# Optimization experiments

Hardware: AMD Instinct MI355X
Metric: run time of the kernel (lower is better)

Reference implementation:

```python
import jax, jax.numpy as jnp
import numpy as np

N_T, N_M, E, Q = 100000, 20000, 600000, 200000
F_IN, D, L = 256, 128, 2


def setup_inputs() -> dict:
    key = jax.random.key(0)
    ks = jax.random.split(key, 20)
    s = 1.0 / np.sqrt(D)
    inp = {
        "x_thesis": jax.random.normal(ks[0], (N_T, F_IN), jnp.float32),
        "mentor_node_id": jnp.arange(N_M, dtype=jnp.int64) if jax.config.jax_enable_x64 else jnp.arange(N_M, dtype=jnp.int32),
        "edge_src": jax.random.randint(ks[1], (E,), 0, N_T),
        "edge_dst": jax.random.randint(ks[2], (E,), 0, N_M),
        "eli_src": jax.random.randint(ks[3], (Q,), 0, N_T),
        "eli_dst": jax.random.randint(ks[4], (Q,), 0, N_M),
        # encoder params
        "thesis_lin_w": jax.random.normal(ks[5], (D, F_IN), jnp.float32) / np.sqrt(F_IN),
        "thesis_lin_b": jnp.zeros((D,), jnp.float32),
        "prof_emb": jax.random.normal(ks[6], (N_M, D), jnp.float32),
        # SAGEConv params per layer, per edge type (sup: thesis->mentor, rev: mentor->thesis)
        "W_nbr_sup": jax.random.normal(ks[7], (L, D, D), jnp.float32) * s,
        "W_root_sup": jax.random.normal(ks[8], (L, D, D), jnp.float32) * s,
        "b_sup": jnp.zeros((L, D), jnp.float32),
        "W_nbr_rev": jax.random.normal(ks[9], (L, D, D), jnp.float32) * s,
        "W_root_rev": jax.random.normal(ks[10], (L, D, D), jnp.float32) * s,
        "b_rev": jnp.zeros((L, D), jnp.float32),
        # classifier Linear(2*D -> 1)
        "cls_w": jax.random.normal(ks[11], (2 * D,), jnp.float32) * (1.0 / np.sqrt(2 * D)),
        "cls_b": jnp.zeros((), jnp.float32),
    }
    return inp


def reference(x_thesis, mentor_node_id, edge_src, edge_dst, eli_src, eli_dst,
              thesis_lin_w, thesis_lin_b, prof_emb,
              W_nbr_sup, W_root_sup, b_sup, W_nbr_rev, W_root_rev, b_rev,
              cls_w, cls_b):
    n_t = x_thesis.shape[0]
    n_m = prof_emb.shape[0]
    L_ = W_nbr_sup.shape[0]

    # node encoders
    h_t = x_thesis @ thesis_lin_w.T + thesis_lin_b          # [N_T, D]
    h_m = prof_emb[mentor_node_id]                          # [N_M, D]

    ones = jnp.ones(edge_src.shape[0], h_t.dtype)
    deg_m = jnp.maximum(jax.ops.segment_sum(ones, edge_dst, num_segments=n_m), 1.0)[:, None]
    deg_t = jnp.maximum(jax.ops.segment_sum(ones, edge_src, num_segments=n_t), 1.0)[:, None]

    for l in range(L_):
        # mean-aggregate thesis feats onto mentors (supervised_by edges)
        agg_m = jax.ops.segment_sum(h_t[edge_src], edge_dst, num_segments=n_m) / deg_m
        # mean-aggregate mentor feats onto theses (reverse edges)
        agg_t = jax.ops.segment_sum(h_m[edge_dst], edge_src, num_segments=n_t) / deg_t
        new_m = agg_m @ W_nbr_sup[l].T + h_m @ W_root_sup[l].T + b_sup[l]
        new_t = agg_t @ W_nbr_rev[l].T + h_t @ W_root_rev[l].T + b_rev[l]
        if l < L_ - 1:
            new_m = jax.nn.relu(new_m)
            new_t = jax.nn.relu(new_t)
        h_t, h_m = new_t, new_m

    # edge-level classifier: gather endpoints, concat, linear -> scalar per pair
    z = jnp.concatenate([h_t[eli_src], h_m[eli_dst]], axis=-1)  # [Q, 2D]
    return z @ cls_w + cls_b                                     # [Q]
```

## Files before the change

### kernel.cpp

```cpp
#include <hip/hip_runtime.h>
#include <cstdint>
#include <cstddef>

#define D 128
#define F_IN 256

typedef __attribute__((ext_vector_type(8))) short bf16x8;
typedef __attribute__((ext_vector_type(4))) float f32x4;

__device__ __forceinline__ unsigned short f2bs(float f) {
  unsigned int x = __builtin_bit_cast(unsigned int, f);
  x = x + 0x7fffu + ((x >> 16) & 1u);
  return (unsigned short)(x >> 16);
}
__device__ __forceinline__ unsigned pk2(float lo, float hi) {
  return (unsigned)f2bs(lo) | ((unsigned)f2bs(hi) << 16);
}
__device__ __forceinline__ float b2f(unsigned int lo16) {
  unsigned int x = lo16 << 16;
  return __builtin_bit_cast(float, x);
}
__device__ __forceinline__ void gl_lds16v(const void* g, void* l) {
  __builtin_amdgcn_global_load_lds(
      (__attribute__((address_space(1))) void*)g,
      (__attribute__((address_space(3))) void*)l, 16, 0, 0);
}
__device__ __forceinline__ uint4 pack8(float4 a, float4 b) {
  uint4 o;
  o.x = pk2(a.x, a.y); o.y = pk2(a.z, a.w);
  o.z = pk2(b.x, b.y); o.w = pk2(b.z, b.w);
  return o;
}


__global__ __launch_bounds__(256) void prep_k(
    const float* __restrict__ s0, unsigned short* __restrict__ d0, int n0,
    const float* __restrict__ s1, unsigned short* __restrict__ d1, int n1,
    const float* __restrict__ s2, unsigned short* __restrict__ d2, int n2,
    const float* __restrict__ s3, unsigned short* __restrict__ d3, int n3,
    const float* __restrict__ s4, unsigned short* __restrict__ d4, int n4,
    int nbC,
    const float* __restrict__ emb, const int* __restrict__ ids,
    unsigned short* __restrict__ hm, int NM, int nbG,
    const int* __restrict__ esrc, const int* __restrict__ edst,
    int* __restrict__ bktT, int* __restrict__ bktM,
    int E, int SHT, int SHM, int nbA)
{
  int bid = blockIdx.x;
  int tid = threadIdx.x;
  if (bid < nbC) {
    int j = bid * 256 + tid;
    const float* s; unsigned short* d;
    if (j < n0) { s = s0; d = d0; }
    else {
      j -= n0;
      if (j < n1) { s = s1; d = d1; }
      else {
        j -= n1;
        if (j < n2) { s = s2; d = d2; }
        else {
          j -= n2;
          if (j < n3) { s = s3; d = d3; }
          else { j -= n3; if (j >= n4) return; s = s4; d = d4; }
        }
      }
    }
    const float4* sp = (const float4*)(s + (size_t)j * 8);
    *(uint4*)(d + (size_t)j * 8) = pack8(sp[0], sp[1]);
    return;
  }
  bid -= nbC;
  if (bid < nbG) {
    int i = bid * 256 + tid;
    if (i >= NM * 16) return;
    int r = i >> 4, c = (i & 15) * 8;
    const float* s = emb + (size_t)ids[r] * D + c;
    *(uint4*)(hm + (size_t)r * D + c) = pack8(*(const float4*)s, *(const float4*)(s + 4));
    return;
  }
  bid -= nbG;
  __shared__ int sh[256];
  sh[tid] = 0;
  __syncthreads();
  int stride = nbA * 256;
  for (int e = bid * 256 + tid; e < E; e += stride) {
    atomicAdd(&sh[esrc[e] >> SHT], 1);
    atomicAdd(&sh[128 + (edst[e] >> SHM)], 1);
  }
  __syncthreads();
  if (tid < 128) { if (sh[tid]) atomicAdd(&bktT[tid], sh[tid]); }
  else { if (sh[tid]) atomicAdd(&bktM[tid - 128], sh[tid]); }
}


__global__ void a2_scan_k(const int* __restrict__ bktT, int* __restrict__ baseT, int* __restrict__ curT, int BT,
                          const int* __restrict__ bktM, int* __restrict__ baseM, int* __restrict__ curM, int BM) {
  __shared__ int sT[129], sM[129];
  int tid = threadIdx.x;
  if (tid < BT) sT[tid] = bktT[tid];
  if (tid < BM) sM[tid] = bktM[tid];
  __syncthreads();
  if (tid == 0) { int r = 0; for (int i = 0; i < BT; ++i) { int c = sT[i]; sT[i] = r; r += c; } sT[BT] = r; }
  if (tid == 1) { int r = 0; for (int i = 0; i < BM; ++i) { int c = sM[i]; sM[i] = r; r += c; } sM[BM] = r; }
  __syncthreads();
  if (tid <= BT) { baseT[tid] = sT[tid]; if (tid < BT) curT[tid] = sT[tid]; }
  if (tid <= BM) { baseM[tid] = sM[tid]; if (tid < BM) curM[tid] = sM[tid]; }
}


#define CH 4096

__device__ __forceinline__ void a3_body(
    const int* __restrict__ esrc, const int* __restrict__ edst,
    unsigned* __restrict__ partT, unsigned* __restrict__ partM,
    int* __restrict__ curT, int* __restrict__ curM,
    int E, int BT, int BM, int SHT, int SHM, int blk, char* smraw)
{
  unsigned* stT = (unsigned*)smraw;
  unsigned* stM = stT + CH;
  int* hT  = (int*)(stM + CH);
  int* lbT = hT + 128;
  int* lcT = hT + 256;
  int* gbT = hT + 384;
  int* hM  = hT + 512;
  int* lbM = hT + 640;
  int* lcM = hT + 768;
  int* gbM = hT + 896;
  int* st2 = hT + 1024;

  int tid = threadIdx.x;
  int c0 = blk * CH;
  int len = E - c0; if (len > CH) len = CH;

  if (tid < 128) { hT[tid] = 0; hM[tid] = 0; }
  __syncthreads();
  for (int i = tid; i < len; i += 256) {
    atomicAdd(&hT[esrc[c0 + i] >> SHT], 1);
    atomicAdd(&hM[edst[c0 + i] >> SHM], 1);
  }
  __syncthreads();
  int own = (tid < 128) ? hT[tid] : hM[tid - 128];
  st2[tid] = own;
  __syncthreads();
  for (int dd = 1; dd < 128; dd <<= 1) {
    int y = ((tid & 127) >= dd) ? st2[tid - dd] : 0;
    __syncthreads();
    st2[tid] += y;
    __syncthreads();
  }
  int excl = st2[tid] - own;
  if (tid < 128) { lbT[tid] = excl; lcT[tid] = excl; }
  else { lbM[tid - 128] = excl; lcM[tid - 128] = excl; }
  __syncthreads();
  if (tid < BT) { if (hT[tid]) gbT[tid] = atomicAdd(&curT[tid], hT[tid]); }
  if (tid >= 128 && tid - 128 < BM) { int m = tid - 128; if (hM[m]) gbM[m] = atomicAdd(&curM[m], hM[m]); }
  __syncthreads();
  for (int i = tid; i < len; i += 256) {
    unsigned s = (unsigned)esrc[c0 + i], dn = (unsigned)edst[c0 + i];
    int p = atomicAdd(&lcT[s >> SHT], 1);
    stT[p] = (s << 15) | dn;
    int q = atomicAdd(&lcM[dn >> SHM], 1);
    stM[q] = (dn << 17) | s;
  }
  __syncthreads();
  for (int b = 0; b < BT; ++b) {
    int cb = hT[b]; if (!cb) continue;
    int lb = lbT[b]; int gb = gbT[b];
    for (int i = tid; i < cb; i += 256) partT[gb + i] = stT[lb + i];
  }
  for (int b = 0; b < BM; ++b) {
    int cb = hM[b]; if (!cb) continue;
    int lb = lbM[b]; int gb = gbM[b];
    for (int i = tid; i < cb; i += 256) partM[gb + i] = stM[lb + i];
  }
}


__device__ __forceinline__ void enc_body(
    const float* __restrict__ A, const unsigned short* __restrict__ W,
    const float* __restrict__ bias, unsigned short* __restrict__ out, int M,
    int blk, char* smraw)
{
  float* bufA0 = (float*)smraw;
  unsigned short* bufW0 = (unsigned short*)(smraw + 32768);
  const int tid = threadIdx.x;
  const int w = tid >> 6, l = tid & 63;
  const int wr = w >> 1, wc = w & 1;
  const int lr = l & 15, kg = l >> 4;
  const int row0 = blk * 128;
  const int arow = l >> 3;
  const int au = l & 7;
  const int wrow = l >> 2;
  const int wu = l & 3;

  f32x4 acc[4][4] = {};

  auto stage = [&](int st, int bsel) {
    int k0 = st * 32;
    float* bA = bufA0 + bsel * 4096;
    unsigned short* bW = bufW0 + bsel * 4096;
#pragma unroll
    for (int q = 0; q < 4; ++q) {
      int r = w * 32 + q * 8 + arow;
      int gr = row0 + r; if (gr >= M) gr = M - 1;
      int gu = au ^ (r & 7);
      gl_lds16v(A + (size_t)gr * F_IN + k0 + gu * 4, bA + (w * 32 + q * 8) * 32 + l * 4);
    }
#pragma unroll
    for (int q = 0; q < 2; ++q) {
      int r = w * 32 + q * 16 + wrow;
      int gu = wu ^ ((r >> 1) & 3);
      gl_lds16v(W + (size_t)r * F_IN + k0 + gu * 8, bW + (w * 32 + q * 16) * 32 + l * 8);
    }
  };

  stage(0, 0);
#pragma unroll 1
  for (int st = 0; st < F_IN / 32; ++st) {
    if (st < F_IN / 32 - 1) {
      stage(st + 1, (st + 1) & 1);
      __builtin_amdgcn_sched_barrier(0);
      asm volatile("s_waitcnt vmcnt(6)" ::: "memory");
    } else {
      __builtin_amdgcn_sched_barrier(0);
      asm volatile("s_waitcnt vmcnt(0)" ::: "memory");
    }
    __builtin_amdgcn_s_barrier();
    __builtin_amdgcn_sched_barrier(0);
    const float* bA = bufA0 + (st & 1) * 4096;
    const unsigned short* bW = bufW0 + (st & 1) * 4096;
    bf16x8 aF[4], bF[4];
#pragma unroll
    for (int i = 0; i < 4; ++i) {
      int r = wr * 64 + i * 16 + lr;
      const float4* pa = (const float4*)(bA + r * 32);
      float4 v0 = pa[(2 * kg) ^ (r & 7)];
      float4 v1 = pa[(2 * kg + 1) ^ (r & 7)];
      uint4 c = pack8(v0, v1);
      aF[i] = *(bf16x8*)&c;
    }
#pragma unroll
    for (int j = 0; j < 4; ++j) {
      int r = wc * 64 + j * 16 + lr;
      bF[j] = *(const bf16x8*)&bW[r * 32 + ((kg ^ ((r >> 1) & 3)) * 8)];
    }
#pragma unroll
    for (int i = 0; i < 4; ++i)
#pragma unroll
      for (int j = 0; j < 4; ++j)
        acc[i][j] = __builtin_amdgcn_mfma_f32_16x16x32_bf16(aF[i], bF[j], acc[i][j], 0, 0, 0);
    __builtin_amdgcn_sched_barrier(0);
    __builtin_amdgcn_s_barrier();
  }

  __syncthreads();
  float bn[4];
#pragma unroll
  for (int j = 0; j < 4; ++j) bn[j] = bias[wc * 64 + j * 16 + lr];
  unsigned short* ow = (unsigned short*)smraw + w * 4096;
#pragma unroll
  for (int i = 0; i < 4; ++i)
#pragma unroll
    for (int j = 0; j < 4; ++j) {
      f32x4 v = acc[i][j];
#pragma unroll
      for (int r = 0; r < 4; ++r)
        ow[(i * 16 + kg * 4 + r) * 64 + j * 16 + lr] = f2bs(v[r] + bn[j]);
    }
  __syncthreads();
#pragma unroll
  for (int q = 0; q < 8; ++q) {
    int u = q * 64 + l;
    int lrow = u >> 3;
    int cu = (u & 7) * 8;
    int gr = row0 + wr * 64 + lrow;
    if (gr < M)
      *(uint4*)(out + (size_t)gr * D + wc * 64 + cu) = *(const uint4*)&ow[lrow * 64 + cu];
  }
}

__global__ __launch_bounds__(256) void a3enc_k(
    const int* __restrict__ esrc, const int* __restrict__ edst,
    unsigned* __restrict__ partT, unsigned* __restrict__ partM,
    int* __restrict__ curT, int* __restrict__ curM,
    int E, int BT, int BM, int SHT, int SHM, int nbA3,
    const float* __restrict__ A, const unsigned short* __restrict__ W,
    const float* __restrict__ bias, unsigned short* __restrict__ out, int M)
{
  __shared__ char smraw[49152];
  if ((int)blockIdx.x < nbA3)
    a3_body(esrc, edst, partT, partM, curT, curM, E, BT, BM, SHT, SHM, blockIdx.x, smraw);
  else
    enc_body(A, W, bias, out, M, blockIdx.x - nbA3, smraw);
}


#define BCAP 12288

__global__ __launch_bounds__(256) void b_csr_k(
    const unsigned* __restrict__ partT, const int* __restrict__ baseT,
    int* __restrict__ rowT, int* __restrict__ csrT, int NT, int BT, int SHT,
    const unsigned* __restrict__ partM, const int* __restrict__ baseM,
    int* __restrict__ rowM, int* __restrict__ csrM, int NM, int BM, int SHM, int E)
{
  __shared__ int cnt[1024];
  __shared__ int st[256];
  __shared__ unsigned stage[BCAP];

  const unsigned* part; const int* base; int* row; int* csr;
  int N, SH, KS; unsigned PM; int b; bool last;
  if ((int)blockIdx.x < BT) {
    part = partT; base = baseT; row = rowT; csr = csrT;
    N = NT; SH = SHT; KS = 15; PM = 0x7fffu; b = blockIdx.x; last = (b == BT - 1);
  } else {
    part = partM; base = baseM; row = rowM; csr = csrM;
    N = NM; SH = SHM; KS = 17; PM = 0x1ffffu; b = blockIdx.x - BT; last = (b == BM - 1);
  }
  int tid = threadIdx.x;
  int ebeg = base[b], eend = base[b + 1];
  int tot = eend - ebeg;
  int n0 = b << SH;
  int width = 1 << SH;
  int nw = N - n0; if (nw > width) nw = width;
  int seg = (width + 255) >> 8;

  for (int j = 0; j < seg; ++j) { int idx = tid * seg + j; if (idx < nw) cnt[idx] = 0; }
  __syncthreads();
  for (int i = tid; i < tot; i += 256) {
    int k = (int)(part[ebeg + i] >> KS) - n0;
    atomicAdd(&cnt[k], 1);
  }
  __syncthreads();
  int s = 0;
  for (int j = 0; j < seg; ++j) { int idx = tid * seg + j; if (idx < nw) s += cnt[idx]; }
  st[tid] = s;
  __syncthreads();
  for (int dd = 1; dd < 256; dd <<= 1) {
    int y = (tid >= dd) ? st[tid - dd] : 0;
    __syncthreads();
    st[tid] += y;
    __syncthreads();
  }
  int run = st[tid] - s;
  for (int j = 0; j < seg; ++j) {
    int idx = tid * seg + j;
    if (idx < nw) {
      int c = cnt[idx];
      row[n0 + idx] = ebeg + run;
      cnt[idx] = run;
      run += c;
    }
  }
  if (last && tid == 0) row[N] = E;
  __syncthreads();
  if (tot <= BCAP) {
    for (int i = tid; i < tot; i += 256) {
      unsigned p = part[ebeg + i];
      int k = (int)(p >> KS) - n0;
      int pos = atomicAdd(&cnt[k], 1);
      stage[pos] = p & PM;
    }
    __syncthreads();
    for (int i = tid; i < tot; i += 256) csr[ebeg + i] = (int)stage[i];
  } else {
    for (int i = tid; i < tot; i += 256) {
      unsigned p = part[ebeg + i];
      int k = (int)(p >> KS) - n0;
      int pos = atomicAdd(&cnt[k], 1);
      csr[ebeg + pos] = (int)(p & PM);
    }
  }
}


__global__ __launch_bounds__(256) void aggregate3_k(
    const unsigned short* __restrict__ tabM, const int* __restrict__ rowpM,
    const int* __restrict__ idxM, unsigned short* __restrict__ outM, int nM, int nblkM,
    const unsigned short* __restrict__ tabT, const int* __restrict__ rowpT,
    const int* __restrict__ idxT, unsigned short* __restrict__ outT, int nT)
{
  const unsigned short* tab; const int* rowp; const int* idx;
  unsigned short* outp; int n, nodeb;
  if ((int)blockIdx.x < nblkM) {
    tab = tabM; rowp = rowpM; idx = idxM; outp = outM; n = nM;
    nodeb = blockIdx.x * 8;
  } else {
    tab = tabT; rowp = rowpT; idx = idxT; outp = outT; n = nT;
    nodeb = (blockIdx.x - nblkM) * 8;
  }
  const int tid = threadIdx.x;
  const int l = tid & 63;
  const int sub = l >> 5;
  const int half = (l >> 4) & 1;
  const int l16 = l & 15;
  const int node = nodeb + (tid >> 6) * 2 + sub;
  const int nodeC = node < n ? node : n - 1;
  int b = rowp[nodeC];
  int e = rowp[nodeC + 1];
  if (node >= n) e = b;
  const int deg = e - b;
  int nb = (deg + 15) >> 4;
  int onb = __shfl_xor(nb, 32, 64);
  int trip = nb > onb ? nb : onb;
  const unsigned short* tl = tab + l16 * 8;

  float a0 = 0.f, a1 = 0.f, a2 = 0.f, a3 = 0.f;
  float a4 = 0.f, a5 = 0.f, a6 = 0.f, a7 = 0.f;
  for (int t = 0; t < trip; ++t) {
    int base = b + t * 16 + half;
    int pp[8]; bool ok[8];
#pragma unroll
    for (int u = 0; u < 8; ++u) {
      int p = base + 2 * u;
      ok[u] = p < e;
      pp[u] = ok[u] ? idx[p] : 0;
    }
    uint4 vv[8];
#pragma unroll
    for (int u = 0; u < 8; ++u) {
      uint4 z; z.x = 0u; z.y = 0u; z.z = 0u; z.w = 0u;
      vv[u] = z;
      if (ok[u]) vv[u] = *(const uint4*)(tl + (size_t)pp[u] * D);
    }
#pragma unroll
    for (int u = 0; u < 8; ++u) {
      a0 += b2f(vv[u].x & 0xffffu); a1 += b2f(vv[u].x >> 16);
      a2 += b2f(vv[u].y & 0xffffu); a3 += b2f(vv[u].y >> 16);
      a4 += b2f(vv[u].z & 0xffffu); a5 += b2f(vv[u].z >> 16);
      a6 += b2f(vv[u].w & 0xffffu); a7 += b2f(vv[u].w >> 16);
    }
  }
  a0 += __shfl_xor(a0, 16, 64);
  a1 += __shfl_xor(a1, 16, 64);
  a2 += __shfl_xor(a2, 16, 64);
  a3 += __shfl_xor(a3, 16, 64);
  a4 += __shfl_xor(a4, 16, 64);
  a5 += __shfl_xor(a5, 16, 64);
  a6 += __shfl_xor(a6, 16, 64);
  a7 += __shfl_xor(a7, 16, 64);
  if (node < n && half == 0) {
    float inv = 1.0f / (float)(deg > 1 ? deg : 1);
    uint4 o;
    o.x = pk2(a0 * inv, a1 * inv);
    o.y = pk2(a2 * inv, a3 * inv);
    o.z = pk2(a4 * inv, a5 * inv);
    o.w = pk2(a6 * inv, a7 * inv);
    *(uint4*)(outp + (size_t)node * D + l16 * 8) = o;
  }
}


template<bool RELU>
__device__ __forceinline__ void gemm_body(
    const unsigned short* __restrict__ Aop, const unsigned short* __restrict__ WA,
    const unsigned short* __restrict__ Bop, const unsigned short* __restrict__ WB,
    const float* __restrict__ bias, unsigned short* __restrict__ out, int M,
    int blk, char* smraw)
{
  unsigned short* bufA0 = (unsigned short*)smraw;
  unsigned short* bufW0 = (unsigned short*)(smraw + 16384);
  const int tid = threadIdx.x;
  const int w = tid >> 6, l = tid & 63;
  const int wr = w >> 1, wc = w & 1;
  const int lr = l & 15, kg = l >> 4;
  const int row0 = blk * 128;
  const int srow = l >> 2;
  const int su = l & 3;

  f32x4 acc[4][4] = {};

  auto stage = [&](int st, int bsel) {
    const unsigned short* Ap = (st < 4) ? Aop : Bop;
    const unsigned short* Wp = (st < 4) ? WA : WB;
    int k0 = (st & 3) * 32;
    unsigned short* bA = bufA0 + bsel * 4096;
    unsigned short* bW = bufW0 + bsel * 4096;
#pragma unroll
    for (int q = 0; q < 2; ++q) {
      int r = w * 32 + q * 16 + srow;
      int gr = row0 + r; if (gr >= M) gr = M - 1;
      int gu = su ^ ((r >> 1) & 3);
      gl_lds16v(Ap + (size_t)gr * D + k0 + gu * 8, bA + (w * 32 + q * 16) * 32 + l * 8);
      gl_lds16v(Wp + (size_t)r * D + k0 + gu * 8, bW + (w * 32 + q * 16) * 32 + l * 8);
    }
  };

  stage(0, 0);
#pragma unroll 1
  for (int st = 0; st < 8; ++st) {
    if (st < 7) {
      stage(st + 1, (st + 1) & 1);
      __builtin_amdgcn_sched_barrier(0);
      asm volatile("s_waitcnt vmcnt(4)" ::: "memory");
    } else {
      __builtin_amdgcn_sched_barrier(0);
      asm volatile("s_waitcnt vmcnt(0)" ::: "memory");
    }
    __builtin_amdgcn_s_barrier();
    __builtin_amdgcn_sched_barrier(0);
    const unsigned short* bA = bufA0 + (st & 1) * 4096;
    const unsigned short* bW = bufW0 + (st & 1) * 4096;
    bf16x8 aF[4], bF[4];
#pragma unroll
    for (int i = 0; i < 4; ++i) {
      int r = wr * 64 + i * 16 + lr;
      aF[i] = *(const bf16x8*)&bA[r * 32 + ((kg ^ ((r >> 1) & 3)) * 8)];
    }
#pragma unroll
    for (int j = 0; j < 4; ++j) {
      int r = wc * 64 + j * 16 + lr;
      bF[j] = *(const bf16x8*)&bW[r * 32 + ((kg ^ ((r >> 1) & 3)) * 8)];
    }
#pragma unroll
    for (int i = 0; i < 4; ++i)
#pragma unroll
      for (int j = 0; j < 4; ++j)
        acc[i][j] = __builtin_amdgcn_mfma_f32_16x16x32_bf16(aF[i], bF[j], acc[i][j], 0, 0, 0);
    __builtin_amdgcn_sched_barrier(0);
    __builtin_amdgcn_s_barrier();
  }

  __syncthreads();
  float bn[4];
#pragma unroll
  for (int j = 0; j < 4; ++j) bn[j] = bias[wc * 64 + j * 16 + lr];
  unsigned short* ow = (unsigned short*)smraw + w * 4096;
#pragma unroll
  for (int i = 0; i < 4; ++i)
#pragma unroll
    for (int j = 0; j < 4; ++j) {
      f32x4 v = acc[i][j];
#pragma unroll
      for (int r = 0; r < 4; ++r) {
        float x = v[r] + bn[j];
        if (RELU) x = fmaxf(x, 0.f);
        ow[(i * 16 + kg * 4 + r) * 64 + j * 16 + lr] = f2bs(x);
      }
    }
  __syncthreads();
#pragma unroll
  for (int q = 0; q < 8; ++q) {
    int u = q * 64 + l;
    int lrow = u >> 3;
    int cu = (u & 7) * 8;
    int gr = row0 + wr * 64 + lrow;
    if (gr < M)
      *(uint4*)(out + (size_t)gr * D + wc * 64 + cu) = *(const uint4*)&ow[lrow * 64 + cu];
  }
}

template<bool RELU>
__global__ __launch_bounds__(256) void gemm_pair_k(
    const unsigned short* __restrict__ Am, const unsigned short* __restrict__ WAm,
    const unsigned short* __restrict__ Bm, const unsigned short* __restrict__ WBm,
    const float* __restrict__ biasm, unsigned short* __restrict__ outm, int Mm, int nbm,
    const unsigned short* __restrict__ At, const unsigned short* __restrict__ WAt,
    const unsigned short* __restrict__ Bt, const unsigned short* __restrict__ WBt,
    const float* __restrict__ biast, unsigned short* __restrict__ outt, int Mt)
{
  __shared__ char smraw[32768];
  if ((int)blockIdx.x < nbm)
    gemm_body<RELU>(Am, WAm, Bm, WBm, biasm, outm, Mm, blockIdx.x, smraw);
  else
    gemm_body<RELU>(At, WAt, Bt, WBt, biast, outt, Mt, blockIdx.x - nbm, smraw);
}


__global__ __launch_bounds__(256) void classify_k(
    const unsigned short* __restrict__ ht, const unsigned short* __restrict__ hm,
    const int* __restrict__ qs, const int* __restrict__ qd,
    const float* __restrict__ w, const float* __restrict__ bptr,
    float* __restrict__ out, int Q)
{
  int g = blockIdx.x * 8 + (threadIdx.x >> 5);
  if (g >= Q) return;
  int l = threadIdx.x & 31;
  const unsigned short* src = (l < 16)
      ? ht + (size_t)qs[g] * D + l * 8
      : hm + (size_t)qd[g] * D + (l - 16) * 8;
  uint4 v = *(const uint4*)src;
  const float* wp = w + l * 8;
  float acc = 0.f;
  acc += b2f(v.x & 0xffffu) * wp[0];
  acc += b2f(v.x >> 16)     * wp[1];
  acc += b2f(v.y & 0xffffu) * wp[2];
  acc += b2f(v.y >> 16)     * wp[3];
  acc += b2f(v.z & 0xffffu) * wp[4];
  acc += b2f(v.z >> 16)     * wp[5];
  acc += b2f(v.w & 0xffffu) * wp[6];
  acc += b2f(v.w >> 16)     * wp[7];
#pragma unroll
  for (int m = 16; m >= 1; m >>= 1) acc += __shfl_xor(acc, m, 64);
  if (l == 0) out[g] = acc + bptr[0];
}


extern "C" void kernel_launch(void* const* d_in, const int* in_sizes, int n_in,
                              void* d_out, int out_size, void* d_ws, size_t ws_size,
                              hipStream_t stream)
{
  const float* x_thesis = (const float*)d_in[0];
  const int*   mentor_id = (const int*)d_in[1];
  const int*   esrc = (const int*)d_in[2];
  const int*   edst = (const int*)d_in[3];
  const int*   qsrc = (const int*)d_in[4];
  const int*   qdst = (const int*)d_in[5];
  const float* lin_w = (const float*)d_in[6];
  const float* lin_b = (const float*)d_in[7];
  const float* prof  = (const float*)d_in[8];
  const float* Wn_sup = (const float*)d_in[9];
  const float* Wr_sup = (const float*)d_in[10];
  const float* b_sup  = (const float*)d_in[11];
  const float* Wn_rev = (const float*)d_in[12];
  const float* Wr_rev = (const float*)d_in[13];
  const float* b_rev  = (const float*)d_in[14];
  const float* cls_w  = (const float*)d_in[15];
  const float* cls_b  = (const float*)d_in[16];

  const int NT = in_sizes[0] / F_IN;
  const int NM = in_sizes[1];
  const int E  = in_sizes[2];
  const int Q  = in_sizes[4];
  const int L  = in_sizes[11] / D;

  int SHT = 0; while ((((NT - 1) >> SHT) + 1) > 128) ++SHT;
  int SHM = 0; while ((((NM - 1) >> SHM) + 1) > 128) ++SHM;
  const int BT = ((NT - 1) >> SHT) + 1;
  const int BM = ((NM - 1) >> SHM) + 1;

  char* wsb = (char*)d_ws;
  size_t off = 0;
  auto alloc = [&](size_t bytes) {
    void* p = wsb + off;
    off = (off + bytes + 255) & ~(size_t)255;
    return p;
  };
  unsigned short* h_t   = (unsigned short*)alloc((size_t)NT * D * 2);
  unsigned short* a_t   = (unsigned short*)alloc((size_t)NT * D * 2);
  unsigned short* h_m   = (unsigned short*)alloc((size_t)NM * D * 2);
  unsigned short* a_m   = (unsigned short*)alloc((size_t)NM * D * 2);
  unsigned short* linw_bf = (unsigned short*)alloc((size_t)D * F_IN * 2);
  unsigned short* wns_bf  = (unsigned short*)alloc((size_t)L * D * D * 2);
  unsigned short* wrs_bf  = (unsigned short*)alloc((size_t)L * D * D * 2);
  unsigned short* wnr_bf  = (unsigned short*)alloc((size_t)L * D * D * 2);
  unsigned short* wrr_bf  = (unsigned short*)alloc((size_t)L * D * D * 2);
  int* row_t = (int*)alloc(((size_t)NT + 1) * 4);
  int* row_m = (int*)alloc(((size_t)NM + 1) * 4);
  int* csr_t = (int*)alloc((size_t)E * 4);
  int* csr_m = (int*)alloc((size_t)E * 4);
  unsigned* partT = (unsigned*)alloc((size_t)E * 4);
  unsigned* partM = (unsigned*)alloc((size_t)E * 4);
  size_t bkt_off = off;
  int* bktT  = (int*)alloc(128 * 4);
  int* bktM  = (int*)alloc(128 * 4);
  size_t bkt_end = off;
  int* baseT = (int*)alloc(129 * 4);
  int* baseM = (int*)alloc(129 * 4);
  int* curT  = (int*)alloc(128 * 4);
  int* curM  = (int*)alloc(128 * 4);
  (void)n_in; (void)out_size; (void)ws_size;

  (void)hipMemsetAsync(wsb + bkt_off, 0, bkt_end - bkt_off, stream);

  {
    int n0 = D * F_IN / 8, nw = L * D * D / 8;
    int totc = n0 + 4 * nw;
    int nbC = (totc + 255) / 256;
    int nbG = (NM * 16 + 255) / 256;
    int nbA = 256;
    prep_k<<<nbC + nbG + nbA, 256, 0, stream>>>(
        lin_w, linw_bf, n0, Wn_sup, wns_bf, nw, Wr_sup, wrs_bf, nw,
        Wn_rev, wnr_bf, nw, Wr_rev, wrr_bf, nw, nbC,
        prof, mentor_id, h_m, NM, nbG,
        esrc, edst, bktT, bktM, E, SHT, SHM, nbA);
  }
  a2_scan_k<<<1, 256, 0, stream>>>(bktT, baseT, curT, BT, bktM, baseM, curM, BM);

  int nbA3 = (E + CH - 1) / CH;
  int nbEnc = (NT + 127) / 128;
  a3enc_k<<<nbA3 + nbEnc, 256, 0, stream>>>(
      esrc, edst, partT, partM, curT, curM, E, BT, BM, SHT, SHM, nbA3,
      x_thesis, linw_bf, lin_b, h_t, NT);

  b_csr_k<<<BT + BM, 256, 0, stream>>>(
      partT, baseT, row_t, csr_t, NT, BT, SHT,
      partM, baseM, row_m, csr_m, NM, BM, SHM, E);

  int agg_nbm = (NM + 7) / 8, agg_nbt = (NT + 7) / 8;
  int gem_nbm = (NM + 127) / 128, gem_nbt = (NT + 127) / 128;
  for (int l = 0; l < L; ++l) {
    aggregate3_k<<<agg_nbm + agg_nbt, 256, 0, stream>>>(
        h_t, row_m, csr_m, a_m, NM, agg_nbm,
        h_m, row_t, csr_t, a_t, NT);

    const unsigned short* wns = wns_bf + (size_t)l * D * D;
    const unsigned short* wrs = wrs_bf + (size_t)l * D * D;
    const unsigned short* wnr = wnr_bf + (size_t)l * D * D;
    const unsigned short* wrr = wrr_bf + (size_t)l * D * D;
    const float* bs = b_sup + (size_t)l * D;
    const float* br = b_rev + (size_t)l * D;
    if (l < L - 1) {
      gemm_pair_k<true><<<gem_nbm + gem_nbt, 256, 0, stream>>>(
          a_m, wns, h_m, wrs, bs, a_m, NM, gem_nbm,
          a_t, wnr, h_t, wrr, br, a_t, NT);
    } else {
      gemm_pair_k<false><<<gem_nbm + gem_nbt, 256, 0, stream>>>(
          a_m, wns, h_m, wrs, bs, a_m, NM, gem_nbm,
          a_t, wnr, h_t, wrr, br, a_t, NT);
    }
    unsigned short* tmp;
    tmp = h_t; h_t = a_t; a_t = tmp;
    tmp = h_m; h_m = a_m; a_m = tmp;
  }

  classify_k<<<(Q + 7) / 8, 256, 0, stream>>>(h_t, h_m, qsrc, qdst, cls_w, cls_b,
                                              (float*)d_out, Q);
}
```

Baseline: 256.8 us.

## Fuse classifier dot product into last-layer GEMM epilogue via per-node scores

Because the classifier is linear over the concatenation, each final node embedding is reduced to a scalar score (dot with the matching half of cls_w) inside the last GEMM's epilogue, using shared-memory atomics per row. The final bf16 embeddings are no longer written, and classification becomes two scalar gathers per query instead of two 256-byte row gathers. This removes the last-layer embedding store and most of the classifier's gather traffic. In exchange it adds LDS atomic contention in the epilogue and keeps scores in fp32 rather than rounding embeddings to bf16, which changes numerics slightly.

```diff
diff --git a/kernel.cpp b/kernel.cpp
--- a/kernel.cpp
+++ b/kernel.cpp
@@ -450,12 +450,13 @@
 }
 
 
-template<bool RELU>
+template<bool RELU, bool LAST>
 __device__ __forceinline__ void gemm_body(
     const unsigned short* __restrict__ Aop, const unsigned short* __restrict__ WA,
     const unsigned short* __restrict__ Bop, const unsigned short* __restrict__ WB,
-    const float* __restrict__ bias, unsigned short* __restrict__ out, int M,
-    int blk, char* smraw)
+    const float* __restrict__ bias, unsigned short* __restrict__ out,
+    float* __restrict__ stout, const float* __restrict__ wcls,
+    int M, int blk, char* smraw)
 {
   unsigned short* bufA0 = (unsigned short*)smraw;
   unsigned short* bufW0 = (unsigned short*)(smraw + 16384);
@@ -524,6 +525,39 @@
   float bn[4];
 #pragma unroll
   for (int j = 0; j < 4; ++j) bn[j] = bias[wc * 64 + j * 16 + lr];
+
+  if (LAST) {
+    float* rowsum = (float*)smraw;
+    if (tid < 128) rowsum[tid] = 0.f;
+    __syncthreads();
+    float wv[4];
+#pragma unroll
+    for (int j = 0; j < 4; ++j) wv[j] = wcls[wc * 64 + j * 16 + lr];
+#pragma unroll
+    for (int i = 0; i < 4; ++i) {
+      float part[4] = {0.f, 0.f, 0.f, 0.f};
+#pragma unroll
+      for (int j = 0; j < 4; ++j) {
+        f32x4 v = acc[i][j];
+#pragma unroll
+        for (int r = 0; r < 4; ++r) {
+          float x = v[r] + bn[j];
+          if (RELU) x = fmaxf(x, 0.f);
+          part[r] += x * wv[j];
+        }
+      }
+#pragma unroll
+      for (int r = 0; r < 4; ++r)
+        atomicAdd(&rowsum[wr * 64 + i * 16 + kg * 4 + r], part[r]);
+    }
+    __syncthreads();
+    if (tid < 128) {
+      int gr = row0 + tid;
+      if (gr < M) stout[gr] = rowsum[tid];
+    }
+    return;
+  }
+
   unsigned short* ow = (unsigned short*)smraw + w * 4096;
 #pragma unroll
   for (int i = 0; i < 4; ++i)
@@ -549,49 +583,32 @@
   }
 }
 
-template<bool RELU>
+template<bool RELU, bool LAST>
 __global__ __launch_bounds__(256) void gemm_pair_k(
     const unsigned short* __restrict__ Am, const unsigned short* __restrict__ WAm,
     const unsigned short* __restrict__ Bm, const unsigned short* __restrict__ WBm,
-    const float* __restrict__ biasm, unsigned short* __restrict__ outm, int Mm, int nbm,
+    const float* __restrict__ biasm, unsigned short* __restrict__ outm,
+    float* __restrict__ stoutm, const float* __restrict__ wclsm, int Mm, int nbm,
     const unsigned short* __restrict__ At, const unsigned short* __restrict__ WAt,
     const unsigned short* __restrict__ Bt, const unsigned short* __restrict__ WBt,
-    const float* __restrict__ biast, unsigned short* __restrict__ outt, int Mt)
+    const float* __restrict__ biast, unsigned short* __restrict__ outt,
+    float* __restrict__ stoutt, const float* __restrict__ wclst, int Mt)
 {
   __shared__ char smraw[32768];
   if ((int)blockIdx.x < nbm)
-    gemm_body<RELU>(Am, WAm, Bm, WBm, biasm, outm, Mm, blockIdx.x, smraw);
+    gemm_body<RELU, LAST>(Am, WAm, Bm, WBm, biasm, outm, stoutm, wclsm, Mm, blockIdx.x, smraw);
   else
-    gemm_body<RELU>(At, WAt, Bt, WBt, biast, outt, Mt, blockIdx.x - nbm, smraw);
-}
-
-
-__global__ __launch_bounds__(256) void classify_k(
-    const unsigned short* __restrict__ ht, const unsigned short* __restrict__ hm,
+    gemm_body<RELU, LAST>(At, WAt, Bt, WBt, biast, outt, stoutt, wclst, Mt, blockIdx.x - nbm, smraw);
+}
+
+
+__global__ __launch_bounds__(256) void classify2_k(
+    const float* __restrict__ st, const float* __restrict__ sm,
     const int* __restrict__ qs, const int* __restrict__ qd,
-    const float* __restrict__ w, const float* __restrict__ bptr,
-    float* __restrict__ out, int Q)
-{
-  int g = blockIdx.x * 8 + (threadIdx.x >> 5);
-  if (g >= Q) return;
-  int l = threadIdx.x & 31;
-  const unsigned short* src = (l < 16)
-      ? ht + (size_t)qs[g] * D + l * 8
-      : hm + (size_t)qd[g] * D + (l - 16) * 8;
-  uint4 v = *(const uint4*)src;
-  const float* wp = w + l * 8;
-  float acc = 0.f;
-  acc += b2f(v.x & 0xffffu) * wp[0];
-  acc += b2f(v.x >> 16)     * wp[1];
-  acc += b2f(v.y & 0xffffu) * wp[2];
-  acc += b2f(v.y >> 16)     * wp[3];
-  acc += b2f(v.z & 0xffffu) * wp[4];
-  acc += b2f(v.z >> 16)     * wp[5];
-  acc += b2f(v.w & 0xffffu) * wp[6];
-  acc += b2f(v.w >> 16)     * wp[7];
-#pragma unroll
-  for (int m = 16; m >= 1; m >>= 1) acc += __shfl_xor(acc, m, 64);
-  if (l == 0) out[g] = acc + bptr[0];
+    const float* __restrict__ bptr, float* __restrict__ out, int Q)
+{
+  int g = blockIdx.x * 256 + threadIdx.x;
+  if (g < Q) out[g] = st[qs[g]] + sm[qd[g]] + bptr[0];
 }
 
 
@@ -639,6 +656,8 @@
   unsigned short* a_t   = (unsigned short*)alloc((size_t)NT * D * 2);
   unsigned short* h_m   = (unsigned short*)alloc((size_t)NM * D * 2);
   unsigned short* a_m   = (unsigned short*)alloc((size_t)NM * D * 2);
+  float* stT = (float*)alloc((size_t)NT * 4);
+  float* smM = (float*)alloc((size_t)NM * 4);
   unsigned short* linw_bf = (unsigned short*)alloc((size_t)D * F_IN * 2);
   unsigned short* wns_bf  = (unsigned short*)alloc((size_t)L * D * D * 2);
   unsigned short* wrs_bf  = (unsigned short*)alloc((size_t)L * D * D * 2);
@@ -700,19 +719,19 @@
     const float* bs = b_sup + (size_t)l * D;
     const float* br = b_rev + (size_t)l * D;
     if (l < L - 1) {
-      gemm_pair_k<true><<<gem_nbm + gem_nbt, 256, 0, stream>>>(
-          a_m, wns, h_m, wrs, bs, a_m, NM, gem_nbm,
-          a_t, wnr, h_t, wrr, br, a_t, NT);
+      gemm_pair_k<true, false><<<gem_nbm + gem_nbt, 256, 0, stream>>>(
+          a_m, wns, h_m, wrs, bs, a_m, nullptr, nullptr, NM, gem_nbm,
+          a_t, wnr, h_t, wrr, br, a_t, nullptr, nullptr, NT);
+      unsigned short* tmp;
+      tmp = h_t; h_t = a_t; a_t = tmp;
+      tmp = h_m; h_m = a_m; a_m = tmp;
     } else {
-      gemm_pair_k<false><<<gem_nbm + gem_nbt, 256, 0, stream>>>(
-          a_m, wns, h_m, wrs, bs, a_m, NM, gem_nbm,
-          a_t, wnr, h_t, wrr, br, a_t, NT);
-    }
-    unsigned short* tmp;
-    tmp = h_t; h_t = a_t; a_t = tmp;
-    tmp = h_m; h_m = a_m; a_m = tmp;
-  }
-
-  classify_k<<<(Q + 7) / 8, 256, 0, stream>>>(h_t, h_m, qsrc, qdst, cls_w, cls_b,
-                                              (float*)d_out, Q);
-}
+      gemm_pair_k<false, true><<<gem_nbm + gem_nbt, 256, 0, stream>>>(
+          a_m, wns, h_m, wrs, bs, nullptr, smM, cls_w + D, NM, gem_nbm,
+          a_t, wnr, h_t, wrr, br, nullptr, stT, cls_w, NT);
+    }
+  }
+
+  classify2_k<<<(Q + 255) / 256, 256, 0, stream>>>(
+      stT, smM, qsrc, qdst, cls_b, (float*)d_out, Q);
+}
```

New measurement: 259.5 us, median of 2. Within noise of the previous version (+1.0%).
